# Optimization experiments

Measured on AMD Instinct MI355X. Metric: run time of the kernel, lower is better.

## Reference

```python
import jax, jax.numpy as jnp
import numpy as np

# uniform-size batching: B graphs, NC compound atoms, NP pocket residues each
B, NC, NP, H = 16, 64, 384, 128
CFEAT, PFEAT = 56, 1280
SCALE = 5.0  # coordinate_scale
LN_EPS = 1e-5


def setup_inputs() -> dict:
    key = jax.random.key(0)
    ks = jax.random.split(key, 16)
    inp = {
        "compound_feats": jax.random.normal(ks[0], (B * NC, CFEAT), jnp.float32),
        "pocket_feats": jax.random.normal(ks[1], (B * NP, PFEAT), jnp.float32),
        "complex_coords": jax.random.normal(ks[2], (B, 2 + NC + NP, 3), jnp.float32) * 10.0,
        "pocket_xyz": jax.random.normal(ks[3], (B, NP, 3), jnp.float32) * 10.0,
        "dis_map": jax.random.uniform(ks[4], (B * NP * NC,), jnp.float32) * 10.0,
        # learned parameters (xavier with gain=0.001 as in the torch init)
        "Wc": jax.random.normal(ks[5], (CFEAT, H), jnp.float32) * 0.001,
        "bc": jnp.zeros((H,), jnp.float32),
        "Wp": jax.random.normal(ks[6], (PFEAT, H), jnp.float32) * 0.001,
        "bp": jnp.zeros((H,), jnp.float32),
        "ln_g": jnp.ones((H,), jnp.float32),
        "ln_b": jnp.zeros((H,), jnp.float32),
        "W1": jax.random.normal(ks[7], (H, H), jnp.float32) * 0.001,
        "b1": jnp.zeros((H,), jnp.float32),
        "W2": jax.random.normal(ks[8], (H, 1), jnp.float32) * 0.001,
        "b2": jnp.zeros((1,), jnp.float32),
    }
    return inp


def _layernorm(x, g, b):
    m = jnp.mean(x, axis=-1, keepdims=True)
    v = jnp.mean(jnp.square(x - m), axis=-1, keepdims=True)
    return (x - m) * jax.lax.rsqrt(v + LN_EPS) * g + b


def reference(compound_feats, pocket_feats, complex_coords, pocket_xyz, dis_map,
              Wc, bc, Wp, bp, ln_g, ln_b, W1, b1, W2, b2):
    norm = lambda x: x / SCALE
    # input linears, then dense-batch (uniform sizes -> exact reshape)
    comp_emb = (compound_feats @ Wc + bc).reshape(B, NC, H)   # [B,NC,H]
    pock_emb = (pocket_feats @ Wp + bp).reshape(B, NP, H)     # [B,NP,H]
    # complex layout per graph: [glb_c, compound (NC), glb_p, pocket (NP)]
    # complex_binding_model treated as identity (see notes): emb/coords pass through.
    comp_coords_out = norm(complex_coords[:, 1:1 + NC])       # [B,NC,3] (normalized)
    pock_coords = norm(pocket_xyz)                            # [B,NP,3]
    # torch.cdist(pocket, compound): [B,NP,NC]
    diff = pock_coords[:, :, None, :] - comp_coords_out[:, None, :, :]
    pc_dis = jnp.sqrt(jnp.sum(jnp.square(diff), axis=-1))
    # layernorm + pairwise outer product + distmap MLP
    p_ln = _layernorm(pock_emb, ln_g, ln_b)
    c_ln = _layernorm(comp_emb, ln_g, ln_b)
    z = jnp.einsum('bik,bjk->bijk', p_ln, c_ln)               # [B,NP,NC,H]
    h = jax.nn.relu(z @ W1 + b1)
    b_logit = (h @ W2 + b2)[..., 0]                            # [B,NP,NC]
    # uniform sizes -> all-true masks, boolean-select is a flatten
    dis_map_pred_by_pair = jax.nn.sigmoid(b_logit.reshape(-1)) * 10.0
    dis_map_pred_by_coord = jnp.clip(pc_dis.reshape(-1) * SCALE, 0.0, 10.0)
    compound_coord_pred = (comp_coords_out * SCALE).reshape(B * NC, 3)
    compound_batch = jnp.repeat(jnp.arange(B, dtype=jnp.int32), NC)
    return (compound_coord_pred, compound_batch, dis_map_pred_by_pair,
            dis_map_pred_by_coord, dis_map)
```

## Files before the change

### kernel.cpp

```cpp
#include <hip/hip_runtime.h>
#include <hip/hip_bf16.h>

#define BB 16
#define NC 64
#define NP 384
#define HH 128
#define CF 56
#define PFT 1280

typedef float f32x4 __attribute__((ext_vector_type(4)));
typedef __bf16 bf16x8 __attribute__((ext_vector_type(8)));
typedef unsigned short u16x8 __attribute__((ext_vector_type(8)));
typedef unsigned short u16x4 __attribute__((ext_vector_type(4)));

static __device__ __forceinline__ unsigned short f2bfu(float f){
  __bf16 h = (__bf16)f;
  return __builtin_bit_cast(unsigned short, h);
}
static __device__ __forceinline__ float bfu2f(unsigned short u){
  __bf16 h = __builtin_bit_cast(__bf16, u);
  return (float)h;
}

__global__ __launch_bounds__(256) void k_prep(
    const float* __restrict__ cf, const float* __restrict__ Wc,
    const float* __restrict__ bc, const float* __restrict__ lng,
    const float* __restrict__ lnb, const float* __restrict__ Wp,
    const float* __restrict__ W1, const float* __restrict__ cc,
    const float* __restrict__ px, const float* __restrict__ dm,
    unsigned short* __restrict__ c_ln, unsigned short* __restrict__ wpt,
    unsigned short* __restrict__ w1t,
    float* __restrict__ out1, float* __restrict__ out4, float* __restrict__ out5){
  __shared__ unsigned short t[128][72];
  __shared__ float redc[2][2], redc2[2][2];
  int bx = blockIdx.x;
  int tid = threadIdx.x;
  if (bx < 20){
    int k0 = bx*64;
    #pragma unroll
    for (int i=0;i<8;i++){
      int fi = tid + i*256;
      int k  = fi>>5;
      int c4 = (fi&31)*4;
      float4 v = *(const float4*)(Wp + (size_t)(k0+k)*HH + c4);
      t[c4+0][k]=f2bfu(v.x); t[c4+1][k]=f2bfu(v.y);
      t[c4+2][k]=f2bfu(v.z); t[c4+3][k]=f2bfu(v.w);
    }
    __syncthreads();
    #pragma unroll
    for (int i=0;i<4;i++){
      int ci = tid + i*256;
      int col = ci>>3, kb = ci&7;
      u16x8 v = *(const u16x8*)&t[col][kb*8];
      *(u16x8*)(wpt + (size_t)col*PFT + k0 + kb*8) = v;
    }
  } else if (bx < 84){
    int idx = (bx-20)*256+tid;
    int k = idx>>7, m = idx&127;
    w1t[m*HH+k] = f2bfu(W1[idx]);
  } else if (bx < 596){
    int rh = tid>>7, m = tid&127;
    int row = (bx-84)*2 + rh;
    const float* cr = cf + row*CF;
    float acc = bc[m];
    #pragma unroll
    for (int k=0;k<CF;k++) acc += cr[k]*Wc[k*HH+m];
    float s=acc, s2=acc*acc;
    #pragma unroll
    for (int off=1; off<64; off<<=1){ s += __shfl_xor(s,off,64); s2 += __shfl_xor(s2,off,64); }
    int wid = (tid>>6)&1;
    if ((m&63)==0){ redc[rh][wid]=s; redc2[rh][wid]=s2; }
    __syncthreads();
    float S=redc[rh][0]+redc[rh][1], S2=redc2[rh][0]+redc2[rh][1];
    float mean = S*(1.0f/HH);
    float var  = S2*(1.0f/HH) - mean*mean;
    float rs = rsqrtf(var + 1e-5f);
    c_ln[(size_t)row*HH+m] = f2bfu((acc-mean)*rs*lng[m] + lnb[m]);
  } else if (bx < 608){
    int idx = (bx-596)*256+tid;
    if (idx < BB*NC*3){
      int bb = idx/(NC*3), rem = idx%(NC*3);
      float v = cc[(size_t)bb*(2+NC+NP)*3 + 3 + rem];
      out1[idx] = (v/5.0f)*5.0f;
    }
    if (idx < BB*NC) out1[BB*NC*3+idx] = (float)(idx>>6);
  } else {
    int idx = (bx-608)*256+tid;
    int b = idx/(NP*NC), r = idx%(NP*NC), i = r>>6, j = r&63;
    const float* pp = px + ((size_t)b*NP+i)*3;
    const float* cp = cc + (size_t)b*(2+NC+NP)*3 + 3 + (size_t)j*3;
    float dx=pp[0]/5.0f-cp[0]/5.0f;
    float dy=pp[1]/5.0f-cp[1]/5.0f;
    float dz=pp[2]/5.0f-cp[2]/5.0f;
    float d = sqrtf(dx*dx+dy*dy+dz*dz)*5.0f;
    d = fminf(fmaxf(d,0.f),10.f);
    out4[idx]=d;
    out5[idx]=dm[idx];
  }
}

__global__ __launch_bounds__(256) void k_main(
    const float* __restrict__ pf, const unsigned short* __restrict__ wpt,
    const float* __restrict__ bp, const float* __restrict__ lng,
    const float* __restrict__ lnb,
    const unsigned short* __restrict__ c_ln, const unsigned short* __restrict__ w1t,
    const float* __restrict__ b1, const float* __restrict__ W2,
    const float* __restrict__ b2p, float* __restrict__ out3){
  __shared__ __align__(16) unsigned short sA[2][16*128];
  __shared__ __align__(16) unsigned short sB[2][HH*128];
  __shared__ __align__(16) float sPf[12*HH];
  int tid = threadIdx.x;
  int w = tid>>6, lane = tid&63, q = lane&15, gr = lane>>4;
  int bx = blockIdx.x;
  int b  = bx>>5;
  int i0 = (bx&31)*12;
  size_t prow0 = (size_t)(b*NP + i0);
  *(unsigned*)((char*)&sA[0][0] + 3072 + tid*4) = 0;
  *(unsigned*)((char*)&sA[1][0] + 3072 + tid*4) = 0;
  f32x4 acc2[2];
  acc2[0]=(f32x4){0.f,0.f,0.f,0.f}; acc2[1]=(f32x4){0.f,0.f,0.f,0.f};
  float4 ra[2]; u16x8 rb[8];
  #define LOADS1(KS) {                                                         \
    int kbase = (KS)*128;                                                      \
    _Pragma("unroll")                                                          \
    for (int i=0;i<2;i++){                                                     \
      int fi = tid + 256*i;                                                    \
      if (fi < 384){                                                           \
        int row = fi>>5, k4 = (fi&31)*4;                                       \
        ra[i] = *(const float4*)(pf + (prow0+row)*PFT + kbase + k4);           \
      }                                                                        \
    }                                                                          \
    _Pragma("unroll")                                                          \
    for (int i=0;i<8;i++){                                                     \
      int ci = tid + 256*i;                                                    \
      int col = ci>>4, kb = ci&15;                                             \
      rb[i] = *(const u16x8*)(wpt + (size_t)col*PFT + kbase + kb*8);           \
    }                                                                          \
  }
  #define WRITES1(BUF) {                                                       \
    char* A = (char*)&sA[BUF][0];                                              \
    char* Bc = (char*)&sB[BUF][0];                                             \
    _Pragma("unroll")                                                          \
    for (int i=0;i<2;i++){                                                     \
      int fi = tid + 256*i;                                                    \
      if (fi < 384){                                                           \
        int row = fi>>5, k4 = (fi&31)*4;                                       \
        u16x4 h = { f2bfu(ra[i].x), f2bfu(ra[i].y), f2bfu(ra[i].z), f2bfu(ra[i].w) }; \
        *(u16x4*)(A + row*256 + (((k4>>3)^(row&15))<<4) + ((k4&7)<<1)) = h;    \
      }                                                                        \
    }                                                                          \
    _Pragma("unroll")                                                          \
    for (int i=0;i<8;i++){                                                     \
      int ci = tid + 256*i;                                                    \
      int col = ci>>4, kb = ci&15;                                             \
      *(u16x8*)(Bc + col*256 + ((kb^(col&15))<<4)) = rb[i];                    \
    }                                                                          \
  }
  LOADS1(0)
  WRITES1(0)
  int cur = 0;
  for (int ks=0; ks<10; ks++){
    if (ks<9) LOADS1(ks+1)
    __syncthreads();
    char* A = (char*)&sA[cur][0];
    char* Bc = (char*)&sB[cur][0];
    #pragma unroll
    for (int kk=0;kk<4;kk++){
      bf16x8 a = *(bf16x8*)(A + q*256 + (((kk*4+gr)^(q&15))<<4));
      #pragma unroll
      for (int ct=0;ct<2;ct++){
        int col = w*32 + ct*16 + q;
        bf16x8 bfr = *(bf16x8*)(Bc + col*256 + (((kk*4+gr)^(col&15))<<4));
        acc2[ct] = __builtin_amdgcn_mfma_f32_16x16x32_bf16(a,bfr,acc2[ct],0,0,0);
      }
    }
    if (ks<9){ WRITES1(cur^1) cur ^= 1; }
  }
  __syncthreads();
  unsigned short* sW = &sB[0][0];
  #pragma unroll
  for (int ct=0;ct<2;ct++){
    int col = w*32 + ct*16 + q;
    float bpv = bp[col];
    #pragma unroll
    for (int r=0;r<4;r++){
      int row = gr*4+r;
      if (row < 12) sPf[row*HH + col] = acc2[ct][r] + bpv;
    }
  }
  {
    const int4* srcW = (const int4*)w1t;
    #pragma unroll
    for (int i=0;i<8;i++){
      int c = tid + 256*i;
      int mm = c>>4, kb = c&15;
      ((int4*)sW)[mm*16 + (kb^(mm&7))] = srcW[c];
    }
  }
  u16x8 cfrag[4];
  {
    const unsigned short* cb = c_ln + (size_t)b*NC*HH + (size_t)(w*16+q)*HH + gr*8;
    #pragma unroll
    for (int kt=0;kt<4;kt++) cfrag[kt] = *(const u16x8*)(cb + kt*32);
  }
  float b1v[8], w2v[8];
  #pragma unroll
  for (int nt=0;nt<8;nt++){ b1v[nt]=b1[nt*16+q]; w2v[nt]=W2[nt*16+q]; }
  float b2 = b2p[0];
  __syncthreads();
  {
    float g0 = lng[lane], g1 = lng[lane+64];
    float B0 = lnb[lane], B1 = lnb[lane+64];
    #pragma unroll
    for (int rr=0; rr<3; rr++){
      int row = w*3+rr;
      float a0 = sPf[row*HH + lane], a1 = sPf[row*HH + lane + 64];
      float s = a0+a1, s2 = a0*a0 + a1*a1;
      #pragma unroll
      for (int off=1; off<64; off<<=1){ s += __shfl_xor(s,off,64); s2 += __shfl_xor(s2,off,64); }
      float mean = s*(1.0f/HH);
      float var  = s2*(1.0f/HH) - mean*mean;
      float rs   = rsqrtf(var + 1e-5f);
      sPf[row*HH + lane]      = (a0-mean)*rs*g0 + B0;
      sPf[row*HH + lane + 64] = (a1-mean)*rs*g1 + B1;
    }
  }
  __syncthreads();
  for (int ii=0; ii<12; ii++){
    f32x4 acc[8];
    #pragma unroll
    for (int nt=0;nt<8;nt++) acc[nt]=(f32x4){0.f,0.f,0.f,0.f};
    #pragma unroll
    for (int kt=0;kt<4;kt++){
      int kblk = kt*4+gr;
      f32x4 p0 = *(const f32x4*)&sPf[ii*HH + kblk*8];
      f32x4 p1 = *(const f32x4*)&sPf[ii*HH + kblk*8 + 4];
      u16x8 cfv = cfrag[kt];
      bf16x8 a;
      #pragma unroll
      for (int e=0;e<4;e++) a[e]   = (__bf16)(bfu2f(cfv[e])*p0[e]);
      #pragma unroll
      for (int e=0;e<4;e++) a[e+4] = (__bf16)(bfu2f(cfv[e+4])*p1[e]);
      #pragma unroll
      for (int nt=0;nt<8;nt++){
        int mm = nt*16+q;
        bf16x8 bv = *(const bf16x8*)&sW[mm*HH + ((kblk^(mm&7))<<3)];
        acc[nt] = __builtin_amdgcn_mfma_f32_16x16x32_bf16(a, bv, acc[nt], 0,0,0);
      }
    }
    float part[4]={0.f,0.f,0.f,0.f};
    #pragma unroll
    for (int nt=0;nt<8;nt++)
      #pragma unroll
      for (int r=0;r<4;r++){
        float h = acc[nt][r] + b1v[nt];
        h = fmaxf(h, 0.f);
        part[r] += h*w2v[nt];
      }
    #pragma unroll
    for (int r=0;r<4;r++){
      part[r]+=__shfl_xor(part[r],1,16);
      part[r]+=__shfl_xor(part[r],2,16);
      part[r]+=__shfl_xor(part[r],4,16);
      part[r]+=__shfl_xor(part[r],8,16);
    }
    if (q==0){
      float4 o;
      o.x = 10.f/(1.f+expf(-(part[0]+b2)));
      o.y = 10.f/(1.f+expf(-(part[1]+b2)));
      o.z = 10.f/(1.f+expf(-(part[2]+b2)));
      o.w = 10.f/(1.f+expf(-(part[3]+b2)));
      *(float4*)(out3 + (prow0+ii)*NC + w*16 + gr*4) = o;
    }
  }
}

extern "C" void kernel_launch(void* const* d_in, const int* in_sizes, int n_in,
                              void* d_out, int out_size, void* d_ws, size_t ws_size,
                              hipStream_t stream){
  const float* cf = (const float*)d_in[0];
  const float* pf = (const float*)d_in[1];
  const float* cc = (const float*)d_in[2];
  const float* px = (const float*)d_in[3];
  const float* dm = (const float*)d_in[4];
  const float* Wc = (const float*)d_in[5];
  const float* bc = (const float*)d_in[6];
  const float* Wp = (const float*)d_in[7];
  const float* bp = (const float*)d_in[8];
  const float* lng= (const float*)d_in[9];
  const float* lnb= (const float*)d_in[10];
  const float* W1 = (const float*)d_in[11];
  const float* b1 = (const float*)d_in[12];
  const float* W2 = (const float*)d_in[13];
  const float* b2 = (const float*)d_in[14];

  float* out = (float*)d_out;
  char* ws = (char*)d_ws;
  unsigned short* c_ln = (unsigned short*)ws;
  unsigned short* w1t  = (unsigned short*)(ws + 262144 + 1572864);
  unsigned short* wpt  = (unsigned short*)(ws + 262144 + 1572864 + 32768);

  float* out1 = out;
  float* out3 = out + BB*NC*3 + BB*NC;
  float* out4 = out3 + BB*NP*NC;
  float* out5 = out4 + BB*NP*NC;

  hipLaunchKernelGGL(k_prep, dim3(2144), dim3(256), 0, stream,
                     cf, Wc, bc, lng, lnb, Wp, W1, cc, px, dm,
                     c_ln, wpt, w1t, out1, out4, out5);
  hipLaunchKernelGGL(k_main, dim3(512), dim3(256), 0, stream,
                     pf, wpt, bp, lng, lnb, c_ln, w1t, b1, W2, b2, out3);
}
```

Measured before the change: 41.84 us.

## Pre-swizzle Wp tiles in prep and stream them to LDS via global_load_lds

```diff
diff --git a/kernel.cpp b/kernel.cpp
--- a/kernel.cpp
+++ b/kernel.cpp
@@ -13,6 +13,9 @@
 typedef unsigned short u16x8 __attribute__((ext_vector_type(8)));
 typedef unsigned short u16x4 __attribute__((ext_vector_type(4)));
 
+typedef __attribute__((address_space(1))) const void glb_void;
+typedef __attribute__((address_space(3))) void lds_void;
+
 static __device__ __forceinline__ unsigned short f2bfu(float f){
   __bf16 h = (__bf16)f;
   return __builtin_bit_cast(unsigned short, h);
@@ -28,7 +31,7 @@
     const float* __restrict__ lnb, const float* __restrict__ Wp,
     const float* __restrict__ W1, const float* __restrict__ cc,
     const float* __restrict__ px, const float* __restrict__ dm,
-    unsigned short* __restrict__ c_ln, unsigned short* __restrict__ wpt,
+    unsigned short* __restrict__ c_ln, unsigned char* __restrict__ wpt,
     unsigned short* __restrict__ w1t,
     float* __restrict__ out1, float* __restrict__ out4, float* __restrict__ out5){
   __shared__ unsigned short t[128][72];
@@ -37,6 +40,7 @@
   int tid = threadIdx.x;
   if (bx < 20){
     int k0 = bx*64;
+    int ks = bx>>1, half = bx&1;
     #pragma unroll
     for (int i=0;i<8;i++){
       int fi = tid + i*256;
@@ -50,9 +54,10 @@
     #pragma unroll
     for (int i=0;i<4;i++){
       int ci = tid + i*256;
-      int col = ci>>3, kb = ci&7;
-      u16x8 v = *(const u16x8*)&t[col][kb*8];
-      *(u16x8*)(wpt + (size_t)col*PFT + k0 + kb*8) = v;
+      int col = ci>>3, kbl = ci&7;
+      int kb = half*8 + kbl;
+      u16x8 v = *(const u16x8*)&t[col][kbl*8];
+      *(u16x8*)(wpt + (size_t)ks*32768 + col*256 + ((kb^(col&15))<<4)) = v;
     }
   } else if (bx < 84){
     int idx = (bx-20)*256+tid;
@@ -100,7 +105,7 @@
 }
 
 __global__ __launch_bounds__(256) void k_main(
-    const float* __restrict__ pf, const unsigned short* __restrict__ wpt,
+    const float* __restrict__ pf, const unsigned char* __restrict__ wpt,
     const float* __restrict__ bp, const float* __restrict__ lng,
     const float* __restrict__ lnb,
     const unsigned short* __restrict__ c_ln, const unsigned short* __restrict__ w1t,
@@ -119,8 +124,16 @@
   *(unsigned*)((char*)&sA[1][0] + 3072 + tid*4) = 0;
   f32x4 acc2[2];
   acc2[0]=(f32x4){0.f,0.f,0.f,0.f}; acc2[1]=(f32x4){0.f,0.f,0.f,0.f};
-  float4 ra[2]; u16x8 rb[8];
-  #define LOADS1(KS) {                                                         \
+  float4 ra[2];
+  #define ISSUEB(KS, BUF) {                                                    \
+    const unsigned char* gb = wpt + (size_t)(KS)*32768 + w*1024 + lane*16;     \
+    unsigned char* lb = (unsigned char*)&sB[BUF][0] + w*1024;                  \
+    _Pragma("unroll")                                                          \
+    for (int i=0;i<8;i++)                                                      \
+      __builtin_amdgcn_global_load_lds(                                        \
+        (glb_void*)(gb + i*4096), (lds_void*)(lb + i*4096), 16, 0, 0);         \
+  }
+  #define LOADA(KS) {                                                          \
     int kbase = (KS)*128;                                                      \
     _Pragma("unroll")                                                          \
     for (int i=0;i<2;i++){                                                     \
@@ -130,16 +143,9 @@
         ra[i] = *(const float4*)(pf + (prow0+row)*PFT + kbase + k4);           \
       }                                                                        \
     }                                                                          \
-    _Pragma("unroll")                                                          \
-    for (int i=0;i<8;i++){                                                     \
-      int ci = tid + 256*i;                                                    \
-      int col = ci>>4, kb = ci&15;                                             \
-      rb[i] = *(const u16x8*)(wpt + (size_t)col*PFT + kbase + kb*8);           \
-    }                                                                          \
-  }
-  #define WRITES1(BUF) {                                                       \
+  }
+  #define WRITEA(BUF) {                                                        \
     char* A = (char*)&sA[BUF][0];                                              \
-    char* Bc = (char*)&sB[BUF][0];                                             \
     _Pragma("unroll")                                                          \
     for (int i=0;i<2;i++){                                                     \
       int fi = tid + 256*i;                                                    \
@@ -149,19 +155,14 @@
         *(u16x4*)(A + row*256 + (((k4>>3)^(row&15))<<4) + ((k4&7)<<1)) = h;    \
       }                                                                        \
     }                                                                          \
-    _Pragma("unroll")                                                          \
-    for (int i=0;i<8;i++){                                                     \
-      int ci = tid + 256*i;                                                    \
-      int col = ci>>4, kb = ci&15;                                             \
-      *(u16x8*)(Bc + col*256 + ((kb^(col&15))<<4)) = rb[i];                    \
-    }                                                                          \
-  }
-  LOADS1(0)
-  WRITES1(0)
+  }
+  ISSUEB(0, 0)
+  LOADA(0)
+  WRITEA(0)
+  __syncthreads();
   int cur = 0;
   for (int ks=0; ks<10; ks++){
-    if (ks<9) LOADS1(ks+1)
-    __syncthreads();
+    if (ks<9){ ISSUEB(ks+1, cur^1) LOADA(ks+1) }
     char* A = (char*)&sA[cur][0];
     char* Bc = (char*)&sB[cur][0];
     #pragma unroll
@@ -174,9 +175,10 @@
         acc2[ct] = __builtin_amdgcn_mfma_f32_16x16x32_bf16(a,bfr,acc2[ct],0,0,0);
       }
     }
-    if (ks<9){ WRITES1(cur^1) cur ^= 1; }
-  }
-  __syncthreads();
+    if (ks<9) WRITEA(cur^1)
+    __syncthreads();
+    cur ^= 1;
+  }
   unsigned short* sW = &sB[0][0];
   #pragma unroll
   for (int ct=0;ct<2;ct++){
@@ -298,7 +300,7 @@
   char* ws = (char*)d_ws;
   unsigned short* c_ln = (unsigned short*)ws;
   unsigned short* w1t  = (unsigned short*)(ws + 262144 + 1572864);
-  unsigned short* wpt  = (unsigned short*)(ws + 262144 + 1572864 + 32768);
+  unsigned char*  wpt  = (unsigned char*)(ws + 262144 + 1572864 + 32768);
 
   float* out1 = out;
   float* out3 = out + BB*NC*3 + BB*NC;
```

After: 42.80 us. +2.3%, slower.
